# Kernel optimization log

Hardware: AMD Instinct MI355X
Metric: run time of the kernel (lower is better)

## Reference

```python
import jax, jax.numpy as jnp
import numpy as np
from jax.scipy.special import i0

# NUFFT adjoint (gridding) configuration, matching m_op.plan(uv, (256,256), (512,512), (6,6))
N = 256          # image side
K = 512
J = 6            # kernel support per dim
B = 8            # batch
M = 100000       # n_measurements
ALPHA = K / N    # oversampling = 2
BETA = float(np.pi * np.sqrt((J / ALPHA * (ALPHA - 0.5)) ** 2 - 0.8))  # Fessler KB beta


def setup_inputs() -> dict:
    key = jax.random.key(0)
    k1, k2, k3, k4 = jax.random.split(key, 4)
    y_real = jax.random.normal(k1, (B, M), dtype=jnp.float32)
    y_imag = jax.random.normal(k2, (B, M), dtype=jnp.float32)
    weights = jax.random.uniform(k3, (M,), dtype=jnp.float32, minval=0.1, maxval=1.0)
    uv = jax.random.uniform(k4, (M, 2), dtype=jnp.float32,
                            minval=-np.pi, maxval=np.pi)
    return {"y_real": y_real, "y_imag": y_imag, "weights": weights, "uv": uv}


def _kb(t):
    # Kaiser-Bessel interpolation kernel, support |t| <= J/2
    u = 2.0 * t / J
    return i0(BETA * jnp.sqrt(jnp.clip(1.0 - u * u, 0.0))) / i0(jnp.asarray(BETA, jnp.float32))


def reference(y_real, y_imag, weights, uv):
    # weighted complex measurements: inputs * measurement_weights
    y = (y_real + 1j * y_imag) * weights[None, :]           # (B, M) complex64

    # map uv in [-pi, pi) to oversampled grid coords in [0, K)
    kf = uv * (K / (2.0 * np.pi))                            # (M, 2), DC at index 0 (mod K)
    base = jnp.floor(kf).astype(jnp.int32)                   # (M, 2)
    offs = jnp.arange(-J // 2 + 1, J // 2 + 1)               # [-2..3], 6 taps
    idx = base[:, :, None] + offs[None, None, :]             # (M, 2, J)
    dist = idx.astype(jnp.float32) - kf[:, :, None]
    w = _kb(dist)                                            # (M, 2, J) separable weights
    idxm = jnp.mod(idx, K)                                   # wrap onto torus

    w2 = (w[:, 0, :, None] * w[:, 1, None, :]).reshape(M, J * J)          # (M, 36)
    lin = (idxm[:, 0, :, None] * K + idxm[:, 1, None, :]).reshape(M * J * J)
    vals = (y[:, :, None] * w2[None, :, :].astype(jnp.complex64)).reshape(B, M * J * J)

    # scatter-add onto oversampled Fourier grid
    grid = jnp.zeros((B, K * K), jnp.complex64).at[:, lin].add(vals)
    grid = grid.reshape(B, K, K)

    # inverse FFT, center, crop to N x N
    img = jnp.fft.fftshift(jnp.fft.ifft2(grid), axes=(1, 2))
    c = K // 2
    img = img[:, c - N // 2:c + N // 2, c - N // 2:c + N // 2]

    # deapodization: divide by 1D FT of the KB kernel (always real here since BETA > pi*J/4*... )
    n = jnp.arange(N, dtype=jnp.float32) - N // 2
    xf = np.pi * J * n / K
    arg = BETA * BETA - xf * xf
    d = jnp.sinh(jnp.sqrt(arg)) / jnp.sqrt(arg)              # (N,)
    apod = d[:, None] * d[None, :]

    x = (jnp.real(img) / apod).astype(jnp.float32)           # tf.math.real(adj_op(...))

    # per-image min-max rescale
    tmax = jnp.max(x, axis=(1, 2), keepdims=True)
    tmin = jnp.min(x, axis=(1, 2), keepdims=True)
    return (x - tmin) / (tmax - tmin)
```

## Files before the change

### kernel.cpp

```cpp
#include <hip/hip_runtime.h>
#include <math.h>

#define NN 256
#define KK 512
#define JJ 6
#define BB 8
#define MPTS 100000
#define NBINS (KK * KK)
#define KF_SCALE 81.48733086305615f

typedef _Float16 h8 __attribute__((ext_vector_type(8)));


__device__ __forceinline__ float i0f_dev(float x) {
    float ax = fabsf(x);
    if (ax < 3.75f) {
        float t = x / 3.75f; t *= t;
        return 1.0f + t*(3.5156229f + t*(3.0899424f + t*(1.2067492f +
               t*(0.2659732f + t*(0.0360768f + t*0.0045813f)))));
    } else {
        float t = 3.75f / ax;
        return (expf(ax) * rsqrtf(ax)) *
               (0.39894228f + t*(0.01328592f + t*(0.00225319f + t*(-0.00157565f +
                t*(0.00916281f + t*(-0.02057706f + t*(0.02635537f +
                t*(-0.01647633f + t*0.00392377f))))))));
    }
}

__device__ __forceinline__ float kbf(float t, float beta, float inv_i0b) {
    float u = t * (1.0f / 3.0f);
    float q = fmaxf(1.0f - u * u, 0.0f);
    return i0f_dev(beta * sqrtf(q)) * inv_i0b;
}

__device__ __forceinline__ unsigned fkey(float f) {
    unsigned u = __float_as_uint(f);
    return (u & 0x80000000u) ? ~u : (u | 0x80000000u);
}
__device__ __forceinline__ float funkey(unsigned k) {
    unsigned u = (k & 0x80000000u) ? (k & 0x7FFFFFFFu) : ~k;
    return __uint_as_float(u);
}


__global__ __launch_bounds__(256) void count_bins(
    const float2* __restrict__ uv2, int* __restrict__ counts)
{
    int m = blockIdx.x * 256 + threadIdx.x;
    if (m >= MPTS) return;
    float2 u = uv2[m];
    int b0 = (int)floorf(u.x * KF_SCALE) & (KK - 1);
    int b1 = (int)floorf(u.y * KF_SCALE) & (KK - 1);
    atomicAdd(&counts[(b0 << 9) | b1], 1);
}

__global__ __launch_bounds__(1024) void scan1(
    const int* __restrict__ counts, int* __restrict__ offsets, int* __restrict__ bsum)
{
    __shared__ int s[1024];
    int i = blockIdx.x * 1024 + threadIdx.x;
    int v = counts[i];
    s[threadIdx.x] = v;
    for (int off = 1; off < 1024; off <<= 1) {
        __syncthreads();
        int t = (threadIdx.x >= off) ? s[threadIdx.x - off] : 0;
        __syncthreads();
        s[threadIdx.x] += t;
    }
    offsets[i] = s[threadIdx.x] - v;
    if (threadIdx.x == 1023) bsum[blockIdx.x] = s[1023];
}

__global__ __launch_bounds__(256) void scan2(
    const int* __restrict__ bsum, int* __restrict__ boff,
    unsigned* __restrict__ mmin, unsigned* __restrict__ mmax)
{
    __shared__ int s[256];
    int v = bsum[threadIdx.x];
    s[threadIdx.x] = v;
    if (threadIdx.x < 8)  mmin[threadIdx.x] = 0xFFFFFFFFu;
    else if (threadIdx.x < 16) mmax[threadIdx.x - 8] = 0u;
    for (int off = 1; off < 256; off <<= 1) {
        __syncthreads();
        int t = (threadIdx.x >= off) ? s[threadIdx.x - off] : 0;
        __syncthreads();
        s[threadIdx.x] += t;
    }
    boff[threadIdx.x] = s[threadIdx.x] - v;
}

__global__ __launch_bounds__(1024) void scan3(
    int* __restrict__ offsets, const int* __restrict__ boff)
{
    int i = blockIdx.x * 1024 + threadIdx.x;
    offsets[i] += boff[blockIdx.x];
    if (i == 0) offsets[NBINS] = MPTS;
}

__global__ __launch_bounds__(256) void fill_records(
    const float2* __restrict__ uv2,
    const float* __restrict__ y_real, const float* __restrict__ y_imag,
    const float* __restrict__ weights, const int* __restrict__ offsets,
    int* __restrict__ counts, char* __restrict__ rec,
    float beta, float inv_i0b)
{
    int m = blockIdx.x * 256 + threadIdx.x;
    if (m >= MPTS) return;
    float2 u = uv2[m];
    float kf0 = u.x * KF_SCALE;
    float kf1 = u.y * KF_SCALE;
    float f0 = floorf(kf0), f1 = floorf(kf1);
    float fr0 = kf0 - f0, fr1 = kf1 - f1;
    int b1c = (int)f1 & (KK - 1);
    int bin = (((int)f0 & (KK - 1)) << 9) | b1c;
    int old = atomicSub(&counts[bin], 1);
    int slot = offsets[bin] + old - 1;

    _Float16 hw[12];
#pragma unroll
    for (int j = 0; j < JJ; ++j) {
        hw[j]     = (_Float16)kbf((float)(j - 2) - fr0, beta, inv_i0b);
        hw[6 + j] = (_Float16)kbf((float)(j - 2) - fr1, beta, inv_i0b);
    }

    float4 c0v, c1v;
    _Float16* p0 = (_Float16*)&c0v;
    _Float16* p1 = (_Float16*)&c1v;
#pragma unroll
    for (int j = 0; j < 8; ++j) p0[j] = hw[j];
#pragma unroll
    for (int j = 0; j < 4; ++j) p1[j] = hw[8 + j];
    ((int*)&c1v)[2] = b1c;
    ((int*)&c1v)[3] = 0;

    float wm = weights[m];
    h8 ha, hb;
#pragma unroll
    for (int b = 0; b < 4; ++b) {
        ha[2 * b]     = (_Float16)(y_real[b * MPTS + m] * wm);
        ha[2 * b + 1] = (_Float16)(y_imag[b * MPTS + m] * wm);
        hb[2 * b]     = (_Float16)(y_real[(b + 4) * MPTS + m] * wm);
        hb[2 * b + 1] = (_Float16)(y_imag[(b + 4) * MPTS + m] * wm);
    }

    float4* dst = (float4*)(rec + (size_t)slot * 64);
    dst[0] = c0v;
    dst[1] = c1v;
    dst[2] = *(float4*)&ha;
    dst[3] = *(float4*)&hb;
}

__global__ __launch_bounds__(256) void gather_grid(
    const int* __restrict__ offsets, const char* __restrict__ rec,
    float* __restrict__ grid)
{
    __shared__ __align__(16) char lds[4][5120];
    int t = threadIdx.x;
    int lane = t & 63;
    int w = t >> 6;
    int j = blockIdx.x;
    int xcd = j & 7;
    int slot = j >> 3;
    int c0 = (xcd << 6) + (slot >> 1);
    int half = slot & 1;
    int c1base = (half << 8) + (w << 6);
    int c1 = c1base + lane;
    int wa = c1 - 3, wb = c1 + 2;

    char* myl = lds[w];

    float aR[BB], aI[BB];
#pragma unroll
    for (int b = 0; b < BB; ++b) { aR[b] = 0.0f; aI[b] = 0.0f; }

    for (int j0 = 0; j0 < JJ; ++j0) {
        int r0 = (c0 - (j0 - 2)) & (KK - 1);
        int rowbase = r0 << 9;
        int lo = c1base - 3, hi = c1base + 65;
        int nseg, ga0, gb0, ga1, gb1;
        if (lo < 0)        { ga0 = lo; gb0 = -1;  ga1 = 0;   gb1 = hi; nseg = 2; }
        else if (hi > 511) { ga0 = lo; gb0 = 511; ga1 = 512; gb1 = hi; nseg = 2; }
        else               { ga0 = lo; gb0 = hi;  ga1 = 0;   gb1 = 0;  nseg = 1; }

        for (int sgi = 0; sgi < nseg; ++sgi) {
            int ga = sgi ? ga1 : ga0;
            int gb = sgi ? gb1 : gb0;
            int pstart = offsets[rowbase + (ga & 511)];
            int pend   = offsets[rowbase + ((gb & 511) + 1)];
            int ia = max(wa, ga), ib = min(wb, gb);
            bool has = ia <= ib;
            int pA = has ? offsets[rowbase + (ia & 511)] : 0;
            int pB = has ? ((ib == gb) ? pend
                                       : offsets[rowbase + ((ib + 1) & 511)]) : 0;

            for (int pc = pstart; pc < pend; pc += 64) {
                int cnt = min(64, pend - pc);
                int sub = lane & 3;
                int prow = lane >> 2;
#pragma unroll
                for (int q = 0; q < 4; ++q) {
                    if (16 * q < cnt) {
                        int pp = min(pc + prow + 16 * q, MPTS - 1);
                        float4 v = *(const float4*)(rec + (size_t)pp * 64 + sub * 16);
                        *(float4*)(myl + (prow + 16 * q) * 80 + sub * 16) = v;
                    }
                }
                int pLo = max(pA, pc), pHi = min(pB, pc + cnt);
                for (int p = pLo; p < pHi; ++p) {
                    const char* rp = myl + (p - pc) * 80;
                    int bin1 = *(const int*)(rp + 24);
                    int idx = (c1 - bin1 + 2) & 511;
                    bool ok = idx <= 5;
                    idx = ok ? idx : 0;
                    float w0 = (float)*(const _Float16*)(rp + j0 * 2);
                    float w1 = (float)*(const _Float16*)(rp + 12 + idx * 2);
                    float ww = ok ? w0 * w1 : 0.0f;
                    h8 ya = *(const h8*)(rp + 32);
                    h8 yb = *(const h8*)(rp + 48);
#pragma unroll
                    for (int b = 0; b < 4; ++b) {
                        aR[b]     += (float)ya[2 * b]     * ww;
                        aI[b]     += (float)ya[2 * b + 1] * ww;
                        aR[b + 4] += (float)yb[2 * b]     * ww;
                        aI[b + 4] += (float)yb[2 * b + 1] * ww;
                    }
                }
            }
        }
    }

    float2* g2 = (float2*)grid;
    int c = (c0 << 9) + c1;
#pragma unroll
    for (int b = 0; b < BB; ++b)
        g2[((size_t)b << 18) + c] = make_float2(aR[b], aI[b]);
}

__device__ __forceinline__ void wave_fft512(float xr[8], float xi[8], int lane)
{
    float a0r = xr[0]+xr[4], a0i = xi[0]+xi[4];
    float a4r = xr[0]-xr[4], a4i = xi[0]-xi[4];
    float a2r = xr[2]+xr[6], a2i = xi[2]+xi[6];
    float a6r = xr[2]-xr[6], a6i = xi[2]-xi[6];
    float a1r = xr[1]+xr[5], a1i = xi[1]+xi[5];
    float a5r = xr[1]-xr[5], a5i = xi[1]-xi[5];
    float a3r = xr[3]+xr[7], a3i = xi[3]+xi[7];
    float a7r = xr[3]-xr[7], a7i = xi[3]-xi[7];
    float b0r = a0r+a2r, b0i = a0i+a2i;
    float b2r = a0r-a2r, b2i = a0i-a2i;
    float b4r = a4r-a6i, b4i = a4i+a6r;
    float b6r = a4r+a6i, b6i = a4i-a6r;
    float b1r = a1r+a3r, b1i = a1i+a3i;
    float b3r = a1r-a3r, b3i = a1i-a3i;
    float b5r = a5r-a7i, b5i = a5i+a7r;
    float b7r = a5r+a7i, b7i = a5i-a7r;
    const float S2 = 0.70710678118654752f;
    float w5r = S2*(b5r-b5i), w5i = S2*(b5r+b5i);
    float w7r = -S2*(b7r+b7i), w7i = S2*(b7r-b7i);
    float y0r = b0r+b1r, y0i = b0i+b1i;
    float y4r = b0r-b1r, y4i = b0i-b1i;
    float y1r = b4r+w5r, y1i = b4i+w5i;
    float y5r = b4r-w5r, y5i = b4i-w5i;
    float y2r = b2r-b3i, y2i = b2i+b3r;
    float y6r = b2r+b3i, y6i = b2i-b3r;
    float y3r = b6r+w7r, y3i = b6i+w7i;
    float y7r = b6r-w7r, y7i = b6i-w7i;

    int p = __brev((unsigned)lane) >> 26;
    float ang = (float)(2.0 * M_PI / 512.0) * (float)p;
    float c1, s1; sincosf(ang, &s1, &c1);
    float wr = c1, wi = s1, tr;
    xr[0] = y0r; xi[0] = y0i;
    xr[1] = y1r*wr - y1i*wi; xi[1] = y1i*wr + y1r*wi;
    tr = wr*c1 - wi*s1; wi = wr*s1 + wi*c1; wr = tr;
    xr[2] = y2r*wr - y2i*wi; xi[2] = y2i*wr + y2r*wi;
    tr = wr*c1 - wi*s1; wi = wr*s1 + wi*c1; wr = tr;
    xr[3] = y3r*wr - y3i*wi; xi[3] = y3i*wr + y3r*wi;
    tr = wr*c1 - wi*s1; wi = wr*s1 + wi*c1; wr = tr;
    xr[4] = y4r*wr - y4i*wi; xi[4] = y4i*wr + y4r*wi;
    tr = wr*c1 - wi*s1; wi = wr*s1 + wi*c1; wr = tr;
    xr[5] = y5r*wr - y5i*wi; xi[5] = y5i*wr + y5r*wi;
    tr = wr*c1 - wi*s1; wi = wr*s1 + wi*c1; wr = tr;
    xr[6] = y6r*wr - y6i*wi; xi[6] = y6i*wr + y6r*wi;
    tr = wr*c1 - wi*s1; wi = wr*s1 + wi*c1; wr = tr;
    xr[7] = y7r*wr - y7i*wi; xi[7] = y7i*wr + y7r*wi;

#pragma unroll
    for (int t = 0; t < 6; ++t) {
        int m = 1 << t;
        int j = lane & (m - 1);
        float wc, wsn;
        sincosf((float)M_PI * (float)j / (float)m, &wsn, &wc);
        bool hi = (lane & m) != 0;
#pragma unroll
        for (int d = 0; d < 8; ++d) {
            float pR = __shfl_xor(xr[d], m, 64);
            float pI = __shfl_xor(xi[d], m, 64);
            float bR = hi ? xr[d] : pR;
            float bI = hi ? xi[d] : pI;
            float aR = hi ? pR : xr[d];
            float aI = hi ? pI : xi[d];
            float wbR = wc * bR - wsn * bI;
            float wbI = wc * bI + wsn * bR;
            xr[d] = hi ? aR - wbR : aR + wbR;
            xi[d] = hi ? aI - wbI : aI + wbI;
        }
    }
}

__global__ __launch_bounds__(512) void fftA(
    const float2* __restrict__ grid2, float2* __restrict__ C)
{
    __shared__ float sR[2112], sI[2112];
    int t = threadIdx.x;
    int lane = t & 63;
    int w = t >> 6;
    int b = blockIdx.x & 7;
    int k1base = (blockIdx.x >> 3) << 3;
    int k1 = k1base + w;

    const float2* row = grid2 + ((size_t)b << 18) + ((size_t)k1 << 9);
    int p = __brev((unsigned)lane) >> 26;
    float xr[8], xi[8];
#pragma unroll
    for (int a = 0; a < 8; ++a) {
        float2 v = row[p + (a << 6)];
        xr[a] = v.x; xi[a] = v.y;
    }

    wave_fft512(xr, xi, lane);

    bool act = (lane < 16) | (lane >= 48);
    int lpp = (lane < 16) ? lane : (lane - 32);
    if (act) {
#pragma unroll
        for (int d = 0; d < 8; ++d) {
            int addr = w * 264 + d * 33 + lpp;
            sR[addr] = xr[d];
            sI[addr] = xi[d];
        }
    }
    __syncthreads();

#pragma unroll
    for (int pp = 0; pp < 4; ++pp) {
        int idx = pp * 512 + t;
        int kk = idx & 7;
        int s2 = idx >> 3;
        int v = (s2 + 128) & 255;
        int d = v & 7;
        int lp = v >> 3;
        int addr = kk * 264 + d * 33 + lp;
        C[(((size_t)(b << 8) + s2) << 9) + k1base + kk] = make_float2(sR[addr], sI[addr]);
    }
}

__global__ __launch_bounds__(256) void fftB(
    const float2* __restrict__ C, float* __restrict__ imgT, float beta2,
    unsigned* __restrict__ mmin, unsigned* __restrict__ mmax)
{
    int t = threadIdx.x;
    int lane = t & 63;
    int w = t >> 6;
    int rowid = blockIdx.x * 4 + w;
    int b = rowid >> 8;
    int s2 = rowid & 255;

    const float2* row = C + ((size_t)rowid << 9);
    int p = __brev((unsigned)lane) >> 26;
    float xr[8], xi[8];
#pragma unroll
    for (int a = 0; a < 8; ++a) {
        float2 v = row[p + (a << 6)];
        xr[a] = v.x; xi[a] = v.y;
    }

    wave_fft512(xr, xi, lane);

    const float XF = (float)(M_PI * (double)JJ / (double)KK);
    const float INVK2 = 1.0f / ((float)KK * (float)KK);
    float ns = (float)(s2 - 128);
    float xfs = XF * ns;
    float asq = beta2 - xfs * xfs;
    float ssq = sqrtf(asq);
    float ds = sinhf(ssq) / ssq;
    float sbase = INVK2 / ds;

    bool act = (lane < 16) | (lane >= 48);
    int lpp = (lane < 16) ? lane : (lane - 32);
    float lmin = 1e30f, lmax = -1e30f;
    if (act) {
        float vals[8];
#pragma unroll
        for (int d = 0; d < 8; ++d) {
            int r = (8 * lpp + d + 128) & 255;
            float nr = (float)(r - 128);
            float xfr = XF * nr;
            float arq = beta2 - xfr * xfr;
            float srq = sqrtf(arq);
            float dr = sinhf(srq) / srq;
            float o = xr[d] * sbase / dr;
            vals[d] = o;
            lmin = fminf(lmin, o);
            lmax = fmaxf(lmax, o);
        }
        int r0run = (8 * lpp + 128) & 255;
        float4* dst = (float4*)(imgT + ((size_t)b << 16) + (s2 << 8) + r0run);
        dst[0] = make_float4(vals[0], vals[1], vals[2], vals[3]);
        dst[1] = make_float4(vals[4], vals[5], vals[6], vals[7]);
    }
#pragma unroll
    for (int off = 32; off >= 1; off >>= 1) {
        lmin = fminf(lmin, __shfl_xor(lmin, off, 64));
        lmax = fmaxf(lmax, __shfl_xor(lmax, off, 64));
    }
    if (lane == 0) {
        atomicMin(&mmin[b], fkey(lmin));
        atomicMax(&mmax[b], fkey(lmax));
    }
}

__global__ __launch_bounds__(256) void norm_t(
    const float* __restrict__ imgT, const unsigned* __restrict__ mmin,
    const unsigned* __restrict__ mmax, float* __restrict__ out)
{
    __shared__ float tile[64][65];
    int b = blockIdx.x >> 4;
    int tl = blockIdx.x & 15;
    int r0 = (tl & 3) << 6;
    int s0 = (tl >> 2) << 6;
    int tr = threadIdx.x & 63;
    int ts = threadIdx.x >> 6;

    const float* src = imgT + ((size_t)b << 16);
#pragma unroll
    for (int q = 0; q < 16; ++q) {
        int s2 = s0 + (q << 2) + ts;
        tile[s2 - s0][tr] = src[(s2 << 8) + r0 + tr];
    }
    __syncthreads();

    float mn = funkey(mmin[b]);
    float inv = 1.0f / (funkey(mmax[b]) - mn);
    float* dst = out + ((size_t)b << 16);
#pragma unroll
    for (int q = 0; q < 16; ++q) {
        int r = r0 + (q << 2) + ts;
        dst[(r << 8) + s0 + tr] = (tile[tr][r - r0] - mn) * inv;
    }
}


static double i0_host(double x) {
    double sum = 1.0, term = 1.0;
    double q = x * x * 0.25;
    for (int k = 1; k < 80; ++k) {
        term *= q / ((double)k * (double)k);
        sum += term;
        if (term < sum * 1e-17) break;
    }
    return sum;
}

extern "C" void kernel_launch(void* const* d_in, const int* in_sizes, int n_in,
                              void* d_out, int out_size, void* d_ws, size_t ws_size,
                              hipStream_t stream)
{
    const float* y_real  = (const float*)d_in[0];
    const float* y_imag  = (const float*)d_in[1];
    const float* weights = (const float*)d_in[2];
    const float* uv      = (const float*)d_in[3];
    float* out = (float*)d_out;

    char* W = (char*)d_ws;
    float*    grid    = (float*)W;
    int*      counts  = (int*)W;
    int*      bsum    = (int*)(W + 0x100000);
    int*      boff    = (int*)(W + 0x100400);
    float*    imgT    = (float*)W;
    char*     A       = W + (size_t)16 * 1024 * 1024;
    char*     rec     = A;
    int*      offsets = (int*)(A + 6400000);
    float2*   C       = (float2*)A;
    unsigned* mmin    = (unsigned*)(A + 8400000);
    unsigned* mmax    = (unsigned*)(A + 8400064);

    double beta_d = M_PI * sqrt(19.45);
    float beta = (float)beta_d;
    float inv_i0b = (float)(1.0 / i0_host(beta_d));
    float beta2 = (float)(beta_d * beta_d);

    hipMemsetAsync(counts, 0, NBINS * sizeof(int), stream);

    count_bins<<<(MPTS + 255) / 256, 256, 0, stream>>>((const float2*)uv, counts);

    scan1<<<256, 1024, 0, stream>>>(counts, offsets, bsum);
    scan2<<<1, 256, 0, stream>>>(bsum, boff, mmin, mmax);
    scan3<<<256, 1024, 0, stream>>>(offsets, boff);

    fill_records<<<(MPTS + 255) / 256, 256, 0, stream>>>(
        (const float2*)uv, y_real, y_imag, weights, offsets, counts,
        rec, beta, inv_i0b);

    gather_grid<<<1024, 256, 0, stream>>>(offsets, rec, grid);

    fftA<<<512, 512, 0, stream>>>((const float2*)grid, C);

    fftB<<<512, 256, 0, stream>>>(C, imgT, beta2, mmin, mmax);

    norm_t<<<128, 256, 0, stream>>>(imgT, mmin, mmax, out);
}
```

Before: 161.6 us.

## Replace three-kernel scan with single-pass decoupled look-back scan

Replaces the scan1/scan2/scan3 sequence with one kernel that uses wave-shuffle scans inside each block and a decoupled look-back over per-block descriptors for the cross-block prefix. The min/max initialisation moves into count_bins, and the descriptor array is zeroed in the same memset as the counts. This removes two kernel launches and the extra pass over the offsets array. The look-back spins on atomics and relies on earlier blocks making progress, which assumes blocks are scheduled roughly in order.

```diff
diff --git a/kernel.cpp b/kernel.cpp
--- a/kernel.cpp
+++ b/kernel.cpp
@@ -42,11 +42,23 @@
     return __uint_as_float(u);
 }
 
+__device__ __forceinline__ int wave_scan(int x, int lane) {
+#pragma unroll
+    for (int off = 1; off < 64; off <<= 1) {
+        int y = __shfl_up(x, off, 64);
+        if (lane >= off) x += y;
+    }
+    return x;
+}
+
 
 __global__ __launch_bounds__(256) void count_bins(
-    const float2* __restrict__ uv2, int* __restrict__ counts)
+    const float2* __restrict__ uv2, int* __restrict__ counts,
+    unsigned* __restrict__ mmin, unsigned* __restrict__ mmax)
 {
     int m = blockIdx.x * 256 + threadIdx.x;
+    if (m < 8) mmin[m] = 0xFFFFFFFFu;
+    else if (m < 16) mmax[m - 8] = 0u;
     if (m >= MPTS) return;
     float2 u = uv2[m];
     int b0 = (int)floorf(u.x * KF_SCALE) & (KK - 1);
@@ -54,47 +66,71 @@
     atomicAdd(&counts[(b0 << 9) | b1], 1);
 }
 
-__global__ __launch_bounds__(1024) void scan1(
-    const int* __restrict__ counts, int* __restrict__ offsets, int* __restrict__ bsum)
-{
-    __shared__ int s[1024];
-    int i = blockIdx.x * 1024 + threadIdx.x;
-    int v = counts[i];
-    s[threadIdx.x] = v;
-    for (int off = 1; off < 1024; off <<= 1) {
-        __syncthreads();
-        int t = (threadIdx.x >= off) ? s[threadIdx.x - off] : 0;
-        __syncthreads();
-        s[threadIdx.x] += t;
-    }
-    offsets[i] = s[threadIdx.x] - v;
-    if (threadIdx.x == 1023) bsum[blockIdx.x] = s[1023];
-}
-
-__global__ __launch_bounds__(256) void scan2(
-    const int* __restrict__ bsum, int* __restrict__ boff,
-    unsigned* __restrict__ mmin, unsigned* __restrict__ mmax)
-{
-    __shared__ int s[256];
-    int v = bsum[threadIdx.x];
-    s[threadIdx.x] = v;
-    if (threadIdx.x < 8)  mmin[threadIdx.x] = 0xFFFFFFFFu;
-    else if (threadIdx.x < 16) mmax[threadIdx.x - 8] = 0u;
-    for (int off = 1; off < 256; off <<= 1) {
-        __syncthreads();
-        int t = (threadIdx.x >= off) ? s[threadIdx.x - off] : 0;
-        __syncthreads();
-        s[threadIdx.x] += t;
-    }
-    boff[threadIdx.x] = s[threadIdx.x] - v;
-}
-
-__global__ __launch_bounds__(1024) void scan3(
-    int* __restrict__ offsets, const int* __restrict__ boff)
-{
-    int i = blockIdx.x * 1024 + threadIdx.x;
-    offsets[i] += boff[blockIdx.x];
-    if (i == 0) offsets[NBINS] = MPTS;
+__global__ __launch_bounds__(1024) void scan_k(
+    const int* __restrict__ counts, int* __restrict__ offsets,
+    unsigned long long* __restrict__ desc)
+{
+    __shared__ int part[16];
+    __shared__ int s_prefix;
+    int tid = threadIdx.x;
+    int lane = tid & 63;
+    int w = tid >> 6;
+    int g = blockIdx.x * 1024 + tid;
+
+    int v = counts[g];
+    int x = wave_scan(v, lane);
+    if (lane == 63) part[w] = x;
+    __syncthreads();
+    if (tid < 16) {
+        int p = part[tid];
+#pragma unroll
+        for (int off = 1; off < 16; off <<= 1) {
+            int y = __shfl_up(p, off, 64);
+            if (tid >= off) p += y;
+        }
+        part[tid] = p;
+    }
+    __syncthreads();
+    int incl = x + ((w > 0) ? part[w - 1] : 0);
+    int total = part[15];
+
+    if (tid == 0) {
+        unsigned long long pack = ((unsigned long long)(unsigned)total << 2) |
+                                  ((blockIdx.x == 0) ? 2ULL : 1ULL);
+        atomicExch(&desc[blockIdx.x], pack);
+        if (blockIdx.x == 0) s_prefix = 0;
+    }
+
+    if (blockIdx.x > 0 && w == 0) {
+        int prefix = 0;
+        int base = blockIdx.x - 1;
+        bool done = false;
+        while (!done) {
+            int idx = base - lane;
+            unsigned long long d = 0;
+            if (idx >= 0) {
+                do { d = atomicAdd(&desc[idx], 0ULL); } while ((d & 3ULL) == 0ULL);
+            }
+            unsigned long long mask = __ballot(idx >= 0 && (d & 3ULL) == 2ULL);
+            int f = (mask != 0ULL) ? (__ffsll((long long)mask) - 1) : 64;
+            int contrib = (idx >= 0 && lane <= f) ? (int)(d >> 2) : 0;
+#pragma unroll
+            for (int off = 1; off < 64; off <<= 1)
+                contrib += __shfl_xor(contrib, off, 64);
+            prefix += contrib;
+            base -= 64;
+            done = (mask != 0ULL);
+        }
+        if (lane == 0) {
+            s_prefix = prefix;
+            atomicExch(&desc[blockIdx.x],
+                       ((unsigned long long)(unsigned)(prefix + total) << 2) | 2ULL);
+        }
+    }
+    __syncthreads();
+
+    offsets[g] = incl - v + s_prefix;
+    if (g == 0) offsets[NBINS] = MPTS;
 }
 
 __global__ __launch_bounds__(256) void fill_records(
@@ -469,14 +505,13 @@
     const float* y_real  = (const float*)d_in[0];
     const float* y_imag  = (const float*)d_in[1];
     const float* weights = (const float*)d_in[2];
-    const float* uv      = (const float*)d_in[3];
+    const float2* uv2    = (const float2*)d_in[3];
     float* out = (float*)d_out;
 
     char* W = (char*)d_ws;
     float*    grid    = (float*)W;
     int*      counts  = (int*)W;
-    int*      bsum    = (int*)(W + 0x100000);
-    int*      boff    = (int*)(W + 0x100400);
+    unsigned long long* desc = (unsigned long long*)(W + 0x100000);
     float*    imgT    = (float*)W;
     char*     A       = W + (size_t)16 * 1024 * 1024;
     char*     rec     = A;
@@ -490,17 +525,15 @@
     float inv_i0b = (float)(1.0 / i0_host(beta_d));
     float beta2 = (float)(beta_d * beta_d);
 
-    hipMemsetAsync(counts, 0, NBINS * sizeof(int), stream);
-
-    count_bins<<<(MPTS + 255) / 256, 256, 0, stream>>>((const float2*)uv, counts);
-
-    scan1<<<256, 1024, 0, stream>>>(counts, offsets, bsum);
-    scan2<<<1, 256, 0, stream>>>(bsum, boff, mmin, mmax);
-    scan3<<<256, 1024, 0, stream>>>(offsets, boff);
+    hipMemsetAsync(counts, 0, NBINS * sizeof(int) + 256 * sizeof(unsigned long long),
+                   stream);
+
+    count_bins<<<(MPTS + 255) / 256, 256, 0, stream>>>(uv2, counts, mmin, mmax);
+
+    scan_k<<<256, 1024, 0, stream>>>(counts, offsets, desc);
 
     fill_records<<<(MPTS + 255) / 256, 256, 0, stream>>>(
-        (const float2*)uv, y_real, y_imag, weights, offsets, counts,
-        rec, beta, inv_i0b);
+        uv2, y_real, y_imag, weights, offsets, counts, rec, beta, inv_i0b);
 
     gather_grid<<<1024, 256, 0, stream>>>(offsets, rec, grid);
 
```

New measurement: 159.5 us. Within noise of the previous version (-1.3%).
